# Kernel optimization log

Measured on AMD Instinct MI355X. Metric: run time of the kernel, lower is better.

## Reference

```python
import jax, jax.numpy as jnp
import numpy as np

B, C, H, W = 64, 32, 112, 112
RANK = 3


def setup_inputs() -> dict:
    key = jax.random.key(0)
    k1, k2, k3, k4, k5 = jax.random.split(key, 5)
    N = H * W  # 12544
    return {
        "x": jax.random.uniform(k1, (B, C, H, W), dtype=jnp.float32),
        "p_buffer": jax.random.normal(k2, (B, N, RANK), dtype=jnp.float32),
        "q_buffer": jax.random.normal(k3, (B, C, RANK), dtype=jnp.float32),
        "grad_p_buffer": jax.random.normal(k4, (B, N, RANK), dtype=jnp.float32),
        "grad_q_buffer": jax.random.normal(k5, (B, C, RANK), dtype=jnp.float32),
        "n_iter": 2,
    }


def _power_svd(X, P, Q, n_iter):
    # X: [b, c, n]; P: [b, n, r]; Q: [b, c, r]
    for i in range(n_iter):
        if i == n_iter - 1:
            P = jnp.linalg.qr(P)[0]  # batched reduced QR, tall-skinny (n x r)
        Q = jnp.einsum('bcn,bnr->bcr', X, P)
        if i == n_iter - 1:
            Q = jnp.linalg.qr(Q)[0]  # batched reduced QR (c x r)
        P = jnp.einsum('bcn,bcr->bnr', X, Q)  # X^T @ Q
    return P, Q


def reference(x, p_buffer, q_buffer, grad_p_buffer, grad_q_buffer, n_iter):
    shape = x.shape
    X = x.reshape(shape[0], shape[1], -1)  # [B, C, H*W]
    P, Q = _power_svd(X, p_buffer, q_buffer, n_iter)
    # low-rank reconstruction Q @ P^T, back to original shape
    return jnp.einsum('bcr,bnr->bcn', Q, P).reshape(shape)
```

## Files before the change

kernel.cpp:

```cpp
#include <hip/hip_runtime.h>
#include <math.h>

#define N_HW 12544
#define TN 256
#define NCHUNK 49

#define WS_QG 65536
#define WS_U  (WS_QG + 64*96)
#define ZTOT  (WS_U)

__device__ __forceinline__ int XQ(int c, int q) {
    return (c << 6) + ((q & ~7) | ((q ^ ((c >> 3) << 1)) & 7));
}

__global__ __launch_bounds__(256)
void k0_zero(float* __restrict__ ws)
{
    const int g = blockIdx.x * 256 + threadIdx.x;
    if (g < ZTOT / 4) ((float4*)ws)[g] = make_float4(0.f, 0.f, 0.f, 0.f);
}

__global__ __launch_bounds__(256)
void k1_gram(const float* __restrict__ x, const float* __restrict__ p,
             float* __restrict__ Sg, float* __restrict__ Qg)
{
    const int b = blockIdx.y, j = blockIdx.x;
    const int tid  = threadIdx.x;
    const int lane = tid & 63, wave = tid >> 6;
    const int nbase = j * TN;

    __shared__ float4 Xs4[32 * 64];
    __shared__ alignas(16) float Ps[TN * 3];
    __shared__ float Qred[8 * 32 * 3];

    {
        const int c = tid >> 3, q0 = tid & 7;
        const float4* xrow = (const float4*)(x + ((size_t)b * 32 + c) * N_HW + nbase);
        #pragma unroll
        for (int k = 0; k < 8; ++k) {
            const int q = q0 + 8 * k;
            Xs4[XQ(c, q)] = xrow[q];
        }
    }
    {
        const float* pb = p + (size_t)b * N_HW * 3 + (size_t)nbase * 3;
        #pragma unroll
        for (int i = 0; i < 3; ++i) Ps[tid + 256 * i] = pb[tid + 256 * i];
    }
    __syncthreads();

    const int sub = lane >> 5, ry = (lane >> 3) & 3, cx = lane & 7;
    const int qbase = wave * 16;
    float acc[8][4] = {};
    for (int t = 0; t < 8; ++t) {
        const int q = qbase + 2 * t + sub;
        float4 bq[4], a[8];
        #pragma unroll
        for (int j2 = 0; j2 < 4; ++j2) bq[j2] = Xs4[XQ(4 * cx + j2, q)];
        #pragma unroll
        for (int i = 0; i < 8; ++i)   a[i]  = Xs4[XQ(8 * ry + i, q)];
        #pragma unroll
        for (int i = 0; i < 8; ++i)
            #pragma unroll
            for (int j2 = 0; j2 < 4; ++j2)
                acc[i][j2] += a[i].x * bq[j2].x + a[i].y * bq[j2].y
                            + a[i].z * bq[j2].z + a[i].w * bq[j2].w;
    }

    {
        const int qc = tid & 31, g = tid >> 5;
        float q0a = 0.f, q1a = 0.f, q2a = 0.f;
        const float4* Ps4 = (const float4*)Ps;
        #pragma unroll
        for (int t = 0; t < 8; ++t) {
            const int q = g * 8 + t;
            float4 xv = Xs4[XQ(qc, q)];
            float4 p0 = Ps4[3 * q], p1 = Ps4[3 * q + 1], p2 = Ps4[3 * q + 2];
            q0a += xv.x * p0.x + xv.y * p0.w + xv.z * p1.z + xv.w * p2.y;
            q1a += xv.x * p0.y + xv.y * p1.x + xv.z * p1.w + xv.w * p2.z;
            q2a += xv.x * p0.z + xv.y * p1.y + xv.z * p2.x + xv.w * p2.w;
        }
        Qred[g * 96 + qc * 3 + 0] = q0a;
        Qred[g * 96 + qc * 3 + 1] = q1a;
        Qred[g * 96 + qc * 3 + 2] = q2a;
    }

    __syncthreads();
    #pragma unroll
    for (int i = 0; i < 8; ++i)
        Xs4[tid * 8 + i] = make_float4(acc[i][0], acc[i][1], acc[i][2], acc[i][3]);
    __syncthreads();

    const float* red = (const float*)Xs4;
    float* Sb = Sg + (size_t)b * 1024;
    #pragma unroll
    for (int it = 0; it < 4; ++it) {
        const int e = tid + 256 * it;
        const int r = e >> 5, cl = e & 31;
        const int ery = r >> 3, ei = r & 7, ecx = cl >> 2, ej = cl & 3;
        const int slot = ery * 8 + ecx;
        float s = 0.f;
        #pragma unroll
        for (int w = 0; w < 4; ++w) {
            s += red[(w * 64 +      slot) * 32 + ei * 4 + ej];
            s += red[(w * 64 + 32 + slot) * 32 + ei * 4 + ej];
        }
        atomicAdd(&Sb[e], s);
    }
    if (tid < 96) {
        float s = 0.f;
        #pragma unroll
        for (int g = 0; g < 8; ++g) s += Qred[g * 96 + tid];
        atomicAdd(&Qg[(size_t)b * 96 + tid], s);
    }
}

__global__ __launch_bounds__(128)
void k2_solve(const float* __restrict__ Sg, const float* __restrict__ Qg,
              float* __restrict__ Uo)
{
    const int b = blockIdx.x, tid = threadIdx.x;
    __shared__ float S[1024];
    __shared__ float Qv[96];
    __shared__ float V[96];
    __shared__ float G[6], L[6];

    #pragma unroll
    for (int i = 0; i < 8; ++i) S[tid + 128 * i] = Sg[(size_t)b * 1024 + tid + 128 * i];
    if (tid < 96) Qv[tid] = Qg[(size_t)b * 96 + tid];
    __syncthreads();
    if (tid < 96) {
        const int c = tid / 3, r = tid % 3;
        float s = 0.f;
        #pragma unroll 8
        for (int cc = 0; cc < 32; ++cc) s += S[c * 32 + cc] * Qv[cc * 3 + r];
        V[tid] = s;
    }
    for (int round = 0; round < 2; ++round) {
        __syncthreads();
        if (tid < 6) {
            const int r = (tid > 2) ? 2 : ((tid > 0) ? 1 : 0);
            const int s = tid - (r * (r + 1)) / 2;
            float g = 0.f;
            for (int c = 0; c < 32; ++c) g += V[c * 3 + r] * V[c * 3 + s];
            G[tid] = g;
        }
        __syncthreads();
        if (tid == 0) {
            const float l00 = sqrtf(G[0]);
            const float l10 = G[1] / l00, l20 = G[3] / l00;
            const float l11 = sqrtf(G[2] - l10 * l10);
            const float l21 = (G[4] - l20 * l10) / l11;
            const float l22 = sqrtf(G[5] - l20 * l20 - l21 * l21);
            L[0] = l00; L[1] = l10; L[2] = l11; L[3] = l20; L[4] = l21; L[5] = l22;
        }
        __syncthreads();
        if (tid < 32) {
            const float v0 = V[tid * 3 + 0], v1 = V[tid * 3 + 1], v2 = V[tid * 3 + 2];
            const float u0 = v0 / L[0];
            const float u1 = (v1 - L[1] * u0) / L[2];
            const float u2 = (v2 - L[3] * u0 - L[4] * u1) / L[5];
            V[tid * 3 + 0] = u0; V[tid * 3 + 1] = u1; V[tid * 3 + 2] = u2;
        }
    }
    __syncthreads();
    if (tid < 32) {
        Uo[(size_t)b * 128 + tid * 4 + 0] = V[tid * 3 + 0];
        Uo[(size_t)b * 128 + tid * 4 + 1] = V[tid * 3 + 1];
        Uo[(size_t)b * 128 + tid * 4 + 2] = V[tid * 3 + 2];
        Uo[(size_t)b * 128 + tid * 4 + 3] = 0.f;
    }
}

__global__ __launch_bounds__(256)
void k3_out(const float* __restrict__ x, const float* __restrict__ Uw,
            float* __restrict__ out)
{
    const int b = blockIdx.y, tid = threadIdx.x;
    __shared__ float Us[32][4];
    if (tid < 128) ((float*)Us)[tid] = Uw[(size_t)b * 128 + tid];
    __syncthreads();
    const int g = blockIdx.x * 256 + tid;
    if (g >= N_HW / 4) return;

    const float* Xb = x   + (size_t)b * 32 * N_HW + 4 * (size_t)g;
    float*       Ob = out + (size_t)b * 32 * N_HW + 4 * (size_t)g;

    float t0x = 0, t0y = 0, t0z = 0, t0w = 0;
    float t1x = 0, t1y = 0, t1z = 0, t1w = 0;
    float t2x = 0, t2y = 0, t2z = 0, t2w = 0;
    #pragma unroll 8
    for (int c = 0; c < 32; ++c) {
        float4 xv = *(const float4*)(Xb + (size_t)c * N_HW);
        const float u0 = Us[c][0], u1 = Us[c][1], u2 = Us[c][2];
        t0x += u0 * xv.x; t0y += u0 * xv.y; t0z += u0 * xv.z; t0w += u0 * xv.w;
        t1x += u1 * xv.x; t1y += u1 * xv.y; t1z += u1 * xv.z; t1w += u1 * xv.w;
        t2x += u2 * xv.x; t2y += u2 * xv.y; t2z += u2 * xv.z; t2w += u2 * xv.w;
    }
    #pragma unroll 8
    for (int c = 0; c < 32; ++c) {
        const float u0 = Us[c][0], u1 = Us[c][1], u2 = Us[c][2];
        float4 o;
        o.x = u0 * t0x + u1 * t1x + u2 * t2x;
        o.y = u0 * t0y + u1 * t1y + u2 * t2y;
        o.z = u0 * t0z + u1 * t1z + u2 * t2z;
        o.w = u0 * t0w + u1 * t1w + u2 * t2w;
        *(float4*)(Ob + (size_t)c * N_HW) = o;
    }
}

extern "C" void kernel_launch(void* const* d_in, const int* in_sizes, int n_in,
                              void* d_out, int out_size, void* d_ws, size_t ws_size,
                              hipStream_t stream)
{
    const float* x = (const float*)d_in[0];
    const float* p = (const float*)d_in[1];
    float* ws = (float*)d_ws;
    float* Sg = ws;
    float* Qg = ws + WS_QG;
    float* U  = ws + WS_U;
    float* out = (float*)d_out;

    hipLaunchKernelGGL(k0_zero, dim3((ZTOT / 4 + 255) / 256), dim3(256), 0, stream, ws);
    hipLaunchKernelGGL(k1_gram, dim3(NCHUNK, 64), dim3(256), 0, stream, x, p, Sg, Qg);
    hipLaunchKernelGGL(k2_solve, dim3(64), dim3(128), 0, stream, Sg, Qg, U);
    hipLaunchKernelGGL(k3_out, dim3((N_HW / 4 + 255) / 256, 64), dim3(256), 0, stream, x, U, out);
}
```

Before: 254.0 us.

## Compute Gram and X·P with bf16x3 split MFMA instead of FP32 FMA

The Gram matrix X·X^T and the X·P product in k1 now run on 32x32x16 bf16 MFMA instructions. Each fp32 value is split into high, mid and low bf16 parts, and several cross products are summed so accuracy stays near fp32. The tile shrinks to 128 columns with twice as many blocks, and the symmetric cross terms are folded in through a transpose during the reduction. k3 also gets larger unrolling and nontemporal output stores. The extra split arithmetic, extra LDS traffic and more atomics may offset the matrix-core gain, and precision depends on the dropped low-order terms.

Measured after the change: 250.3 us. Within noise of the previous version (-1.5%).

```diff
diff --git a/kernel.cpp b/kernel.cpp
--- a/kernel.cpp
+++ b/kernel.cpp
@@ -2,15 +2,33 @@
 #include <math.h>
 
 #define N_HW 12544
-#define TN 256
-#define NCHUNK 49
+#define TN 128
+#define NCH 98
 
 #define WS_QG 65536
 #define WS_U  (WS_QG + 64*96)
 #define ZTOT  (WS_U)
 
-__device__ __forceinline__ int XQ(int c, int q) {
-    return (c << 6) + ((q & ~7) | ((q ^ ((c >> 3) << 1)) & 7));
+typedef __attribute__((ext_vector_type(8)))  short short8;
+typedef __attribute__((ext_vector_type(16))) float f32x16;
+typedef __attribute__((ext_vector_type(4)))  float f32x4;
+
+#define MFMA(a, b, c) __builtin_amdgcn_mfma_f32_32x32x16_bf16((a), (b), (c), 0, 0, 0)
+
+__device__ __forceinline__ void split3(float f, ushort& h, ushort& m, ushort& l) {
+    unsigned u = __builtin_bit_cast(unsigned, f);
+    h = (ushort)(u >> 16);
+    float fh = __builtin_bit_cast(float, u & 0xffff0000u);
+    float rm = f - fh;
+    unsigned um = __builtin_bit_cast(unsigned, rm);
+    m = (ushort)(um >> 16);
+    float fm = __builtin_bit_cast(float, um & 0xffff0000u);
+    float rl = rm - fm;
+    l = (ushort)(__builtin_bit_cast(unsigned, rl) >> 16);
+}
+
+__device__ __forceinline__ int xq(int c, int o) {
+    return c * 16 + ((o & 8) | ((o ^ c) & 7));
 }
 
 __global__ __launch_bounds__(256)
@@ -25,92 +43,119 @@
              float* __restrict__ Sg, float* __restrict__ Qg)
 {
     const int b = blockIdx.y, j = blockIdx.x;
-    const int tid  = threadIdx.x;
+    const int tid = threadIdx.x;
     const int lane = tid & 63, wave = tid >> 6;
     const int nbase = j * TN;
 
-    __shared__ float4 Xs4[32 * 64];
-    __shared__ alignas(16) float Ps[TN * 3];
-    __shared__ float Qred[8 * 32 * 3];
+    __shared__ uint4 XS[3 * 512];
+    __shared__ alignas(16) ushort PTH[3 * TN], PTM[3 * TN], PTL[3 * TN];
+    __shared__ float Ssum[1024], T2[1024], T3[1024];
+    float* dmp = (float*)XS;
 
     {
-        const int c = tid >> 3, q0 = tid & 7;
-        const float4* xrow = (const float4*)(x + ((size_t)b * 32 + c) * N_HW + nbase);
+        const int c = tid >> 3, oc = tid & 7;
+        const float4* xr = (const float4*)(x + ((size_t)b * 32 + c) * N_HW + nbase);
         #pragma unroll
-        for (int k = 0; k < 8; ++k) {
-            const int q = q0 + 8 * k;
-            Xs4[XQ(c, q)] = xrow[q];
-        }
-    }
+        for (int t = 0; t < 2; ++t) {
+            const int o = oc + 8 * t;
+            float4 f0 = xr[2 * o], f1 = xr[2 * o + 1];
+            float fv[8] = {f0.x, f0.y, f0.z, f0.w, f1.x, f1.y, f1.z, f1.w};
+            unsigned hw[4], mw[4], lw[4];
+            #pragma unroll
+            for (int i = 0; i < 4; ++i) {
+                ushort h0, m0, l0, h1, m1, l1;
+                split3(fv[2 * i],     h0, m0, l0);
+                split3(fv[2 * i + 1], h1, m1, l1);
+                hw[i] = (unsigned)h0 | ((unsigned)h1 << 16);
+                mw[i] = (unsigned)m0 | ((unsigned)m1 << 16);
+                lw[i] = (unsigned)l0 | ((unsigned)l1 << 16);
+            }
+            const int s = xq(c, o);
+            XS[s]        = make_uint4(hw[0], hw[1], hw[2], hw[3]);
+            XS[512 + s]  = make_uint4(mw[0], mw[1], mw[2], mw[3]);
+            XS[1024 + s] = make_uint4(lw[0], lw[1], lw[2], lw[3]);
+        }
+    }
+    if (tid < TN) {
+        const float* pb = p + (size_t)b * N_HW * 3 + (size_t)(nbase + tid) * 3;
+        #pragma unroll
+        for (int r = 0; r < 3; ++r) {
+            ushort h, m, l;
+            split3(pb[r], h, m, l);
+            PTH[r * TN + tid] = h; PTM[r * TN + tid] = m; PTL[r * TN + tid] = l;
+        }
+    }
+    __syncthreads();
+
+    f32x16 D1 = {0,0,0,0,0,0,0,0,0,0,0,0,0,0,0,0};
+    f32x16 D2 = {0,0,0,0,0,0,0,0,0,0,0,0,0,0,0,0};
+    f32x16 D3 = {0,0,0,0,0,0,0,0,0,0,0,0,0,0,0,0};
+    f32x16 DQ = {0,0,0,0,0,0,0,0,0,0,0,0,0,0,0,0};
+    const int cl = lane & 31, g = lane >> 5;
+    const int rr = (cl < 3) ? cl : 0;
+    for (int s = wave; s < 8; s += 4) {
+        const int sl = xq(cl, 2 * s + g);
+        short8 xh = __builtin_bit_cast(short8, XS[sl]);
+        short8 xm = __builtin_bit_cast(short8, XS[512 + sl]);
+        short8 xl = __builtin_bit_cast(short8, XS[1024 + sl]);
+        const int po = rr * TN + 16 * s + 8 * g;
+        short8 ph = *(const short8*)&PTH[po];
+        short8 pm = *(const short8*)&PTM[po];
+        short8 pl = *(const short8*)&PTL[po];
+        D1 = MFMA(xh, xh, D1);
+        D1 = MFMA(xm, xm, D1);
+        D2 = MFMA(xh, xm, D2);
+        D3 = MFMA(xh, xl, D3);
+        DQ = MFMA(xh, ph, DQ);
+        DQ = MFMA(xh, pm, DQ);
+        DQ = MFMA(xm, ph, DQ);
+        DQ = MFMA(xh, pl, DQ);
+        DQ = MFMA(xl, ph, DQ);
+        DQ = MFMA(xm, pm, DQ);
+    }
+
+    #define DUMP_REDUCE(D, dst)                                                            \
+        __syncthreads();                                                                   \
+        _Pragma("unroll")                                                                  \
+        for (int i = 0; i < 4; ++i)                                                        \
+            *(float4*)&dmp[tid * 20 + 4 * i] =                                             \
+                make_float4((D)[4*i], (D)[4*i+1], (D)[4*i+2], (D)[4*i+3]);                 \
+        __syncthreads();                                                                   \
+        _Pragma("unroll")                                                                  \
+        for (int it = 0; it < 4; ++it) {                                                   \
+            const int e = tid + 256 * it;                                                  \
+            const int r = e >> 5, co = e & 31;                                             \
+            const int ln = co + 32 * ((r >> 2) & 1);                                       \
+            const int rg = (r & 3) + 4 * (r >> 3);                                         \
+            (dst)[e] = dmp[ln * 20 + rg] + dmp[(64 + ln) * 20 + rg]                        \
+                     + dmp[(128 + ln) * 20 + rg] + dmp[(192 + ln) * 20 + rg];              \
+        }
+
+    DUMP_REDUCE(D1, Ssum)
+    DUMP_REDUCE(D2, T2)
+    DUMP_REDUCE(D3, T3)
+    __syncthreads();
     {
-        const float* pb = p + (size_t)b * N_HW * 3 + (size_t)nbase * 3;
+        float* Sb = Sg + (size_t)b * 1024;
         #pragma unroll
-        for (int i = 0; i < 3; ++i) Ps[tid + 256 * i] = pb[tid + 256 * i];
-    }
-    __syncthreads();
-
-    const int sub = lane >> 5, ry = (lane >> 3) & 3, cx = lane & 7;
-    const int qbase = wave * 16;
-    float acc[8][4] = {};
-    for (int t = 0; t < 8; ++t) {
-        const int q = qbase + 2 * t + sub;
-        float4 bq[4], a[8];
-        #pragma unroll
-        for (int j2 = 0; j2 < 4; ++j2) bq[j2] = Xs4[XQ(4 * cx + j2, q)];
-        #pragma unroll
-        for (int i = 0; i < 8; ++i)   a[i]  = Xs4[XQ(8 * ry + i, q)];
-        #pragma unroll
-        for (int i = 0; i < 8; ++i)
-            #pragma unroll
-            for (int j2 = 0; j2 < 4; ++j2)
-                acc[i][j2] += a[i].x * bq[j2].x + a[i].y * bq[j2].y
-                            + a[i].z * bq[j2].z + a[i].w * bq[j2].w;
-    }
-
-    {
-        const int qc = tid & 31, g = tid >> 5;
-        float q0a = 0.f, q1a = 0.f, q2a = 0.f;
-        const float4* Ps4 = (const float4*)Ps;
-        #pragma unroll
-        for (int t = 0; t < 8; ++t) {
-            const int q = g * 8 + t;
-            float4 xv = Xs4[XQ(qc, q)];
-            float4 p0 = Ps4[3 * q], p1 = Ps4[3 * q + 1], p2 = Ps4[3 * q + 2];
-            q0a += xv.x * p0.x + xv.y * p0.w + xv.z * p1.z + xv.w * p2.y;
-            q1a += xv.x * p0.y + xv.y * p1.x + xv.z * p1.w + xv.w * p2.z;
-            q2a += xv.x * p0.z + xv.y * p1.y + xv.z * p2.x + xv.w * p2.w;
-        }
-        Qred[g * 96 + qc * 3 + 0] = q0a;
-        Qred[g * 96 + qc * 3 + 1] = q1a;
-        Qred[g * 96 + qc * 3 + 2] = q2a;
-    }
-
+        for (int it = 0; it < 4; ++it) {
+            const int e = tid + 256 * it;
+            const int r = e >> 5, co = e & 31;
+            const int et = (co << 5) | r;
+            atomicAdd(&Sb[e], Ssum[e] + T2[e] + T2[et] + T3[e] + T3[et]);
+        }
+    }
     __syncthreads();
     #pragma unroll
-    for (int i = 0; i < 8; ++i)
-        Xs4[tid * 8 + i] = make_float4(acc[i][0], acc[i][1], acc[i][2], acc[i][3]);
-    __syncthreads();
-
-    const float* red = (const float*)Xs4;
-    float* Sb = Sg + (size_t)b * 1024;
-    #pragma unroll
-    for (int it = 0; it < 4; ++it) {
-        const int e = tid + 256 * it;
-        const int r = e >> 5, cl = e & 31;
-        const int ery = r >> 3, ei = r & 7, ecx = cl >> 2, ej = cl & 3;
-        const int slot = ery * 8 + ecx;
-        float s = 0.f;
-        #pragma unroll
-        for (int w = 0; w < 4; ++w) {
-            s += red[(w * 64 +      slot) * 32 + ei * 4 + ej];
-            s += red[(w * 64 + 32 + slot) * 32 + ei * 4 + ej];
-        }
-        atomicAdd(&Sb[e], s);
-    }
+    for (int i = 0; i < 4; ++i)
+        *(float4*)&dmp[tid * 20 + 4 * i] = make_float4(DQ[4*i], DQ[4*i+1], DQ[4*i+2], DQ[4*i+3]);
+    __syncthreads();
     if (tid < 96) {
-        float s = 0.f;
-        #pragma unroll
-        for (int g = 0; g < 8; ++g) s += Qred[g * 96 + tid];
+        const int c2 = tid / 3, r2 = tid - 3 * c2;
+        const int ln = r2 + 32 * ((c2 >> 2) & 1);
+        const int rg = (c2 & 3) + 4 * (c2 >> 3);
+        float s = dmp[ln * 20 + rg] + dmp[(64 + ln) * 20 + rg]
+                + dmp[(128 + ln) * 20 + rg] + dmp[(192 + ln) * 20 + rg];
         atomicAdd(&Qg[(size_t)b * 96 + tid], s);
     }
 }
@@ -189,7 +234,7 @@
     float t0x = 0, t0y = 0, t0z = 0, t0w = 0;
     float t1x = 0, t1y = 0, t1z = 0, t1w = 0;
     float t2x = 0, t2y = 0, t2z = 0, t2w = 0;
-    #pragma unroll 8
+    #pragma unroll 16
     for (int c = 0; c < 32; ++c) {
         float4 xv = *(const float4*)(Xb + (size_t)c * N_HW);
         const float u0 = Us[c][0], u1 = Us[c][1], u2 = Us[c][2];
@@ -197,15 +242,15 @@
         t1x += u1 * xv.x; t1y += u1 * xv.y; t1z += u1 * xv.z; t1w += u1 * xv.w;
         t2x += u2 * xv.x; t2y += u2 * xv.y; t2z += u2 * xv.z; t2w += u2 * xv.w;
     }
-    #pragma unroll 8
+    #pragma unroll 16
     for (int c = 0; c < 32; ++c) {
         const float u0 = Us[c][0], u1 = Us[c][1], u2 = Us[c][2];
-        float4 o;
+        f32x4 o;
         o.x = u0 * t0x + u1 * t1x + u2 * t2x;
         o.y = u0 * t0y + u1 * t1y + u2 * t2y;
         o.z = u0 * t0z + u1 * t1z + u2 * t2z;
         o.w = u0 * t0w + u1 * t1w + u2 * t2w;
-        *(float4*)(Ob + (size_t)c * N_HW) = o;
+        __builtin_nontemporal_store(o, (f32x4*)(Ob + (size_t)c * N_HW));
     }
 }
 
@@ -222,7 +267,7 @@
     float* out = (float*)d_out;
 
     hipLaunchKernelGGL(k0_zero, dim3((ZTOT / 4 + 255) / 256), dim3(256), 0, stream, ws);
-    hipLaunchKernelGGL(k1_gram, dim3(NCHUNK, 64), dim3(256), 0, stream, x, p, Sg, Qg);
+    hipLaunchKernelGGL(k1_gram, dim3(NCH, 64), dim3(256), 0, stream, x, p, Sg, Qg);
     hipLaunchKernelGGL(k2_solve, dim3(64), dim3(128), 0, stream, Sg, Qg, U);
     hipLaunchKernelGGL(k3_out, dim3((N_HW / 4 + 255) / 256, 64), dim3(256), 0, stream, x, U, out);
 }
```
